# Performance work log

Hardware: AMD Instinct MI355X
Metric: run time of the kernel (lower is better)

Reference implementation:

```python
import jax, jax.numpy as jnp
import numpy as np

EMBED = 768
HEADS = 12
HEAD_DIM = EMBED // HEADS
HIDDEN = 3072
EPS = 1e-5


def setup_inputs() -> dict:
    key = jax.random.key(0)
    ks = jax.random.split(key, 8)
    s = lambda d: 1.0 / np.sqrt(d)
    return {
        "x": jax.random.normal(ks[0], (1, 4096, EMBED), jnp.float32),
        "ln1_w": jnp.ones((EMBED,), jnp.float32),
        "ln1_b": jnp.zeros((EMBED,), jnp.float32),
        "qkv_w": jax.random.normal(ks[1], (3 * EMBED, EMBED), jnp.float32) * s(EMBED),
        "qkv_b": jnp.zeros((3 * EMBED,), jnp.float32),
        "out_w": jax.random.normal(ks[2], (EMBED, EMBED), jnp.float32) * s(EMBED),
        "out_b": jnp.zeros((EMBED,), jnp.float32),
        "ln2_w": jnp.ones((EMBED,), jnp.float32),
        "ln2_b": jnp.zeros((EMBED,), jnp.float32),
        "fc1_w": jax.random.normal(ks[3], (HIDDEN, EMBED), jnp.float32) * s(EMBED),
        "fc1_b": jnp.zeros((HIDDEN,), jnp.float32),
        "fc2_w": jax.random.normal(ks[4], (EMBED, HIDDEN), jnp.float32) * s(HIDDEN),
        "fc2_b": jnp.zeros((EMBED,), jnp.float32),
    }


def _layernorm(x, w, b):
    mu = jnp.mean(x, axis=-1, keepdims=True)
    var = jnp.mean(jnp.square(x - mu), axis=-1, keepdims=True)
    return (x - mu) * jax.lax.rsqrt(var + EPS) * w + b


def reference(x, ln1_w, ln1_b, qkv_w, qkv_b, out_w, out_b,
              ln2_w, ln2_b, fc1_w, fc1_b, fc2_w, fc2_b):
    B, N, _ = x.shape
    # attention branch
    h = _layernorm(x, ln1_w, ln1_b)
    qkv = h @ qkv_w.T + qkv_b                      # [B,N,3E]
    qkv = qkv.reshape(B, N, 3, HEADS, HEAD_DIM)
    q = jnp.transpose(qkv[:, :, 0], (0, 2, 1, 3))  # [B,H,N,D]
    k = jnp.transpose(qkv[:, :, 1], (0, 2, 1, 3))
    v = jnp.transpose(qkv[:, :, 2], (0, 2, 1, 3))
    scores = jnp.einsum("bhqd,bhkd->bhqk", q, k) / np.sqrt(HEAD_DIM)
    probs = jax.nn.softmax(scores, axis=-1)
    attn = jnp.einsum("bhqk,bhkd->bhqd", probs, v)
    attn = jnp.transpose(attn, (0, 2, 1, 3)).reshape(B, N, EMBED)
    x = x + (attn @ out_w.T + out_b)
    # mlp branch
    h = _layernorm(x, ln2_w, ln2_b)
    h = jax.nn.gelu(h @ fc1_w.T + fc1_b, approximate=False)
    x = x + (h @ fc2_w.T + fc2_b)
    return x
```

## Files before the change

kernel.cpp:

```cpp
#include <hip/hip_runtime.h>
#include <hip/hip_bf16.h>

#define SEQ  4096
#define EMB  768
#define NH   12
#define HD   64
#define HID  3072
#define QKVC 2304

typedef __attribute__((ext_vector_type(8))) short bf16x8;
typedef __attribute__((ext_vector_type(4))) float f32x4;

#define MFMA16(a,b,c) __builtin_amdgcn_mfma_f32_16x16x32_bf16(a,b,c,0,0,0)

#define QSCL 0.18033688f

__device__ __forceinline__ unsigned short f2bf(float f){
  union { float f; unsigned u; } c; c.f = f;
  unsigned r = c.u + 0x7FFFu + ((c.u >> 16) & 1u);
  return (unsigned short)(r >> 16);
}

__device__ __forceinline__ float bf2f(unsigned short u){
  union { unsigned u; float f; } c; c.u = (unsigned)u << 16; return c.f;
}

__device__ __forceinline__ unsigned cvtpk(float a, float b){
  unsigned r;
  asm("v_cvt_pk_bf16_f32 %0, %1, %2" : "=v"(r) : "v"(a), "v"(b));
  return r;
}

__device__ __forceinline__ float gelu_f(float x){
  float x2 = x * x;
  float u  = __builtin_amdgcn_exp2f(x * fmaf(x2, 0.1029433f, 2.3022082f));
  return x * u * __builtin_amdgcn_rcpf(1.f + u);
}

__device__ __forceinline__ void gload_lds16(const unsigned short* g, unsigned short* l){
  __builtin_amdgcn_global_load_lds(
      (const __attribute__((address_space(1))) unsigned int*)g,
      (__attribute__((address_space(3))) unsigned int*)l, 16, 0, 0);
}

__global__ void cvt4_kernel(const float* __restrict__ s0, unsigned short* __restrict__ d0, int n0,
                            const float* __restrict__ s1, unsigned short* __restrict__ d1, int n1,
                            const float* __restrict__ s2, unsigned short* __restrict__ d2, int n2,
                            const float* __restrict__ s3, unsigned short* __restrict__ d3, int n3){
  long e = ((long)blockIdx.x * 256 + threadIdx.x) << 2;
  const float* s; unsigned short* d;
  if (e < n0){ s = s0; d = d0; }
  else if ((e -= n0) < n1){ s = s1; d = d1; }
  else if ((e -= n1) < n2){ s = s2; d = d2; }
  else if ((e -= n2) < n3){ s = s3; d = d3; }
  else return;
  float4 v = *(const float4*)(s + e);
  ushort4 u;
  u.x = f2bf(v.x); u.y = f2bf(v.y); u.z = f2bf(v.z); u.w = f2bf(v.w);
  *(ushort4*)(d + e) = u;
}

__global__ __launch_bounds__(256) void ln_kernel(const float* __restrict__ x,
    const float* __restrict__ w, const float* __restrict__ b,
    unsigned short* __restrict__ out)
{
  const int row = blockIdx.x;
  const float* xr = x + (size_t)row * EMB;
  const int t = threadIdx.x;
  float v0 = xr[t], v1 = xr[t + 256], v2 = xr[t + 512];
  float s  = v0 + v1 + v2;
  float s2 = v0*v0 + v1*v1 + v2*v2;
  #pragma unroll
  for (int off = 32; off; off >>= 1){ s += __shfl_down(s, off); s2 += __shfl_down(s2, off); }
  __shared__ float rs[4], rq[4], st[2];
  int wv = t >> 6;
  if ((t & 63) == 0){ rs[wv] = s; rq[wv] = s2; }
  __syncthreads();
  if (t == 0){
    float S  = rs[0] + rs[1] + rs[2] + rs[3];
    float S2 = rq[0] + rq[1] + rq[2] + rq[3];
    float mu  = S * (1.f / 768.f);
    float var = S2 * (1.f / 768.f) - mu * mu;
    st[0] = mu; st[1] = rsqrtf(var + 1e-5f);
  }
  __syncthreads();
  float mu = st[0], rstd = st[1];
  unsigned short* orow = out + (size_t)row * EMB;
  orow[t]       = f2bf((v0 - mu) * rstd * w[t]       + b[t]);
  orow[t + 256] = f2bf((v1 - mu) * rstd * w[t + 256] + b[t + 256]);
  orow[t + 512] = f2bf((v2 - mu) * rstd * w[t + 512] + b[t + 512]);
}

template<int EPI, int BM, int BN, int BK>
__global__ __launch_bounds__(256, (BM == 64 ? 4 : 3)) void gemm_kernel(
    const unsigned short* __restrict__ A, const unsigned short* __restrict__ B,
    const float* __restrict__ bias, const float* __restrict__ res,
    unsigned short* __restrict__ Ob, float* __restrict__ Of,
    int M, int N, int K)
{
  constexpr int MF  = BM / 32;
  constexpr int NF  = BN / 32;
  constexpr int KS  = BK / 32;
  constexpr int CPR = BK / 8;
  constexpr int AIT = BM * BK / 2048;
  constexpr int BIT = BN * BK / 2048;
  __shared__ unsigned short sA[2][BM * BK];
  __shared__ unsigned short sB[2][BN * BK];
  const int tid  = threadIdx.x;
  const int w    = tid >> 6, lane = tid & 63;
  const int wr   = w >> 1,   wc   = w & 1;
  const int l15  = lane & 15, l4  = lane >> 4;
  const int tm   = blockIdx.y, tn = blockIdx.x;
  const unsigned short* Ab = A + (size_t)tm * BM * K;
  const unsigned short* Bb = B + (size_t)tn * BN * K;

  f32x4 acc[MF][NF];
  #pragma unroll
  for (int m = 0; m < MF; ++m)
    #pragma unroll
    for (int n = 0; n < NF; ++n){ acc[m][n][0]=0.f; acc[m][n][1]=0.f; acc[m][n][2]=0.f; acc[m][n][3]=0.f; }

  #define GSTAGE(buf, kt) { \
    const int k0_ = (kt) * BK; \
    _Pragma("unroll") \
    for (int i = 0; i < AIT; ++i){ \
      int c = i * 256 + tid; int row = c / CPR; int skc = (c % CPR) ^ (row & (CPR - 1)); \
      gload_lds16(Ab + (size_t)row * K + k0_ + skc * 8, &sA[buf][(i * 256 + w * 64) * 8]); } \
    _Pragma("unroll") \
    for (int i = 0; i < BIT; ++i){ \
      int c = i * 256 + tid; int row = c / CPR; int skc = (c % CPR) ^ (row & (CPR - 1)); \
      gload_lds16(Bb + (size_t)row * K + k0_ + skc * 8, &sB[buf][(i * 256 + w * 64) * 8]); }}

  #define GCOMPUTE(buf) { \
    _Pragma("unroll") \
    for (int ks = 0; ks < KS; ++ks){ \
      bf16x8 af[MF], bg[NF]; \
      _Pragma("unroll") \
      for (int m = 0; m < MF; ++m){ \
        int row = wr * (BM / 2) + m * 16 + l15; \
        int kc  = ks * 4 + l4; \
        af[m] = *(const bf16x8*)&sA[buf][row * BK + ((kc ^ (row & (CPR - 1))) << 3)]; } \
      _Pragma("unroll") \
      for (int n = 0; n < NF; ++n){ \
        int row = wc * (BN / 2) + n * 16 + l15; \
        int kc  = ks * 4 + l4; \
        bg[n] = *(const bf16x8*)&sB[buf][row * BK + ((kc ^ (row & (CPR - 1))) << 3)]; } \
      _Pragma("unroll") \
      for (int m = 0; m < MF; ++m) \
        _Pragma("unroll") \
        for (int n = 0; n < NF; ++n) \
          acc[m][n] = MFMA16(af[m], bg[n], acc[m][n]); }}

  const int nk = K / BK;
  GSTAGE(0, 0);
  int cur = 0;
  for (int kt = 0; kt < nk; ++kt){
    __syncthreads();
    if (kt + 1 < nk) GSTAGE(cur ^ 1, kt + 1);
    GCOMPUTE(cur);
    cur ^= 1;
  }
  #undef GSTAGE
  #undef GCOMPUTE

  #pragma unroll
  for (int m = 0; m < MF; ++m){
    int row0 = tm * BM + wr * (BM / 2) + m * 16 + l4 * 4;
    #pragma unroll
    for (int n = 0; n < NF; ++n){
      int col = tn * BN + wc * (BN / 2) + n * 16 + l15;
      float bv = bias[col];
      #pragma unroll
      for (int r = 0; r < 4; ++r){
        int row = row0 + r;
        float v = acc[m][n][r] + bv;
        if (EPI == 0){
          Ob[(size_t)row * N + col] = f2bf(v);
        } else if (EPI == 1){
          Ob[(size_t)row * N + col] = f2bf(gelu_f(v));
        } else if (EPI == 3){
          if (col < EMB) v *= QSCL;
          Ob[(size_t)row * N + col] = f2bf(v);
        } else {
          v += res[(size_t)row * N + col];
          Of[(size_t)row * N + col] = v;
        }
      }
    }
  }
}

__global__ __launch_bounds__(256, 3) void attn_kernel(
    const unsigned short* __restrict__ qkv,
    unsigned short* __restrict__ pO, float2* __restrict__ pml)
{
  __shared__ unsigned short sK[2][64 * 64];
  __shared__ unsigned short sVt[2][64 * 64];
  __shared__ unsigned short sEp[4][16 * 72];
  const int tid = threadIdx.x, w = tid >> 6, lane = tid & 63;
  const int l15 = lane & 15, l4 = lane >> 4;

  const int bid  = blockIdx.x;
  const int v_id = (bid & 7) * 96 + (bid >> 3);
  const int head = v_id >> 6;
  const int r6   = v_id & 63;
  const int qt   = r6 >> 1;
  const int sk   = r6 & 1;

  const int koff = EMB + head * HD;
  const int voff = 2 * EMB + head * HD;
  const int qbase = qt * 128 + w * 32;
  const int tbase = sk * 32;

  bf16x8 qf[2][2];
  #pragma unroll
  for (int qg = 0; qg < 2; ++qg){
    const unsigned short* qp = qkv + (size_t)(qbase + qg * 16 + l15) * QKVC + head * HD + l4 * 8;
    qf[qg][0] = *(const bf16x8*)qp;
    qf[qg][1] = *(const bf16x8*)(qp + 32);
  }

  f32x4 oaccT[4][2];
  #pragma unroll
  for (int i = 0; i < 4; ++i)
    #pragma unroll
    for (int qg = 0; qg < 2; ++qg){ oaccT[i][qg][0]=0.f; oaccT[i][qg][1]=0.f; oaccT[i][qg][2]=0.f; oaccT[i][qg][3]=0.f; }
  float m0 = -3.0e38f, m1 = -3.0e38f, l0 = 0.f, l1 = 0.f;

  const int krow = tid >> 3;
  const int kskc = (tid & 7) ^ (krow & 7);
  const int vp_  = tid >> 3;
  const int d0   = (tid & 7) * 8;
  const int w16  = vp_ & 15;
  const int qpos = (w16 & 1) | (((w16 >> 3) & 1) << 1) | (((w16 >> 1) & 3) << 2);
  const int Pc   = ((vp_ >> 4) << 2) | (qpos >> 2);
  const int Ps   = qpos & 3;

  #define KSTAGE(buf, t) { \
    const int kv0_ = (t) << 6; \
    gload_lds16(qkv + (size_t)(kv0_ + krow) * QKVC + koff + kskc * 8,      &sK[buf][(w * 64) * 8]); \
    gload_lds16(qkv + (size_t)(kv0_ + 32 + krow) * QKVC + koff + kskc * 8, &sK[buf][(256 + w * 64) * 8]); }

  #define VLOAD(t) { \
    const unsigned short* vp = qkv + (size_t)(((t) << 6) + vp_ * 2) * QKVC + voff + d0; \
    va = *(const bf16x8*)vp; \
    vb = *(const bf16x8*)(vp + QKVC); }

  #define VCOMMIT(buf) { \
    _Pragma("unroll") \
    for (int i = 0; i < 8; ++i){ \
      unsigned pk = (unsigned)(unsigned short)va[i] | ((unsigned)(unsigned short)vb[i] << 16); \
      *(unsigned*)&sVt[buf][(d0 + i) * 64 + ((Pc ^ (tid & 7) ^ i) << 3) + Ps * 2] = pk; \
    } }

  bf16x8 va, vb;
  KSTAGE(0, tbase);
  VLOAD(tbase);
  VCOMMIT(0);

  for (int tt = 0; tt < 32; ++tt){
    const int cur = tt & 1;
    __syncthreads();
    const bool pre = (tt < 31);
    if (pre){
      KSTAGE(cur ^ 1, tbase + tt + 1);
      VLOAD(tbase + tt + 1);
    }

    f32x4 sf[4][2];
    #pragma unroll
    for (int i = 0; i < 4; ++i)
      #pragma unroll
      for (int qg = 0; qg < 2; ++qg){ sf[i][qg][0]=0.f; sf[i][qg][1]=0.f; sf[i][qg][2]=0.f; sf[i][qg][3]=0.f; }
    __builtin_amdgcn_s_setprio(1);
    #pragma unroll
    for (int ks = 0; ks < 2; ++ks){
      bf16x8 kf[4];
      #pragma unroll
      for (int nb = 0; nb < 4; ++nb){
        int row = 16 * nb + l15;
        kf[nb] = *(const bf16x8*)&sK[cur][(row * 8 + ((4 * ks + l4) ^ (row & 7))) * 8];
      }
      #pragma unroll
      for (int nb = 0; nb < 4; ++nb){
        sf[nb][0] = MFMA16(kf[nb], qf[0][ks], sf[nb][0]);
        sf[nb][1] = MFMA16(kf[nb], qf[1][ks], sf[nb][1]);
      }
    }
    __builtin_amdgcn_s_setprio(0);

    float mx0, mx1;
    {
      float a = sf[0][0][0], b = sf[0][1][0];
      #pragma unroll
      for (int nb = 0; nb < 4; ++nb)
        #pragma unroll
        for (int r = 0; r < 4; ++r){
          a = fmaxf(a, sf[nb][0][r]);
          b = fmaxf(b, sf[nb][1][r]);
        }
      a = fmaxf(a, __shfl_xor(a, 16)); a = fmaxf(a, __shfl_xor(a, 32));
      b = fmaxf(b, __shfl_xor(b, 16)); b = fmaxf(b, __shfl_xor(b, 32));
      mx0 = a; mx1 = b;
    }
    bool ok = (mx0 <= m0 + 8.f) && (mx1 <= m1 + 8.f);
    if (!__all(ok)){
      float nm0 = fmaxf(m0, mx0), nm1 = fmaxf(m1, mx1);
      float c0 = __builtin_amdgcn_exp2f(m0 - nm0);
      float c1 = __builtin_amdgcn_exp2f(m1 - nm1);
      m0 = nm0; m1 = nm1; l0 *= c0; l1 *= c1;
      #pragma unroll
      for (int db = 0; db < 4; ++db)
        #pragma unroll
        for (int r = 0; r < 4; ++r){ oaccT[db][0][r] *= c0; oaccT[db][1][r] *= c1; }
    }
    unsigned pbw[2][2][4];
    {
      float ps0 = 0.f, ps1 = 0.f;
      #pragma unroll
      for (int nb = 0; nb < 4; ++nb){
        float p0[4], p1[4];
        #pragma unroll
        for (int r = 0; r < 4; ++r){
          p0[r] = __builtin_amdgcn_exp2f(sf[nb][0][r] - m0); ps0 += p0[r];
          p1[r] = __builtin_amdgcn_exp2f(sf[nb][1][r] - m1); ps1 += p1[r];
        }
        pbw[0][nb >> 1][(nb & 1) * 2]     = cvtpk(p0[0], p0[1]);
        pbw[0][nb >> 1][(nb & 1) * 2 + 1] = cvtpk(p0[2], p0[3]);
        pbw[1][nb >> 1][(nb & 1) * 2]     = cvtpk(p1[0], p1[1]);
        pbw[1][nb >> 1][(nb & 1) * 2 + 1] = cvtpk(p1[2], p1[3]);
      }
      ps0 += __shfl_xor(ps0, 16); ps0 += __shfl_xor(ps0, 32);
      ps1 += __shfl_xor(ps1, 16); ps1 += __shfl_xor(ps1, 32);
      l0 += ps0; l1 += ps1;
    }

    __builtin_amdgcn_s_setprio(1);
    {
      bf16x8 vv[2][4];
      #pragma unroll
      for (int ks = 0; ks < 2; ++ks)
        #pragma unroll
        for (int db = 0; db < 4; ++db){
          int d = 16 * db + l15;
          int cp = (4 * ks + l4) ^ ((d >> 3) & 7) ^ (d & 7);
          vv[ks][db] = *(const bf16x8*)&sVt[cur][d * 64 + cp * 8];
        }
      union { unsigned uw[4]; bf16x8 v; } pb;
      #pragma unroll
      for (int qg = 0; qg < 2; ++qg){
        bf16x8 pb0, pb1;
        pb.uw[0]=pbw[qg][0][0]; pb.uw[1]=pbw[qg][0][1]; pb.uw[2]=pbw[qg][0][2]; pb.uw[3]=pbw[qg][0][3]; pb0 = pb.v;
        pb.uw[0]=pbw[qg][1][0]; pb.uw[1]=pbw[qg][1][1]; pb.uw[2]=pbw[qg][1][2]; pb.uw[3]=pbw[qg][1][3]; pb1 = pb.v;
        #pragma unroll
        for (int db = 0; db < 4; ++db){
          oaccT[db][qg] = MFMA16(vv[0][db], pb0, oaccT[db][qg]);
          oaccT[db][qg] = MFMA16(vv[1][db], pb1, oaccT[db][qg]);
        }
      }
    }
    __builtin_amdgcn_s_setprio(0);

    if (pre) VCOMMIT(cur ^ 1);
  }

  #pragma unroll
  for (int qg = 0; qg < 2; ++qg){
    unsigned short* sPw = sEp[w];
    #pragma unroll
    for (int db = 0; db < 4; ++db)
      #pragma unroll
      for (int dw = 0; dw < 2; ++dw){
        unsigned pk = cvtpk(oaccT[db][qg][2 * dw], oaccT[db][qg][2 * dw + 1]);
        *(unsigned*)&sPw[l15 * 72 + 16 * db + 4 * l4 + 2 * dw] = pk;
      }
    int qe = lane >> 2, de = (lane & 3) * 16;
    bf16x8 r0 = *(const bf16x8*)&sPw[qe * 72 + de];
    bf16x8 r1 = *(const bf16x8*)&sPw[qe * 72 + de + 8];
    unsigned short* op = pO + ((size_t)(sk * NH + head) * SEQ + qbase + qg * 16 + qe) * 64 + de;
    *(bf16x8*)op = r0;
    *(bf16x8*)(op + 8) = r1;
  }
  if (lane < 16){
    size_t r = (size_t)(sk * NH + head) * SEQ + qbase + l15;
    pml[r]      = make_float2(m0, l0);
    pml[r + 16] = make_float2(m1, l1);
  }
  #undef KSTAGE
  #undef VLOAD
  #undef VCOMMIT
}

__global__ __launch_bounds__(256) void comb_kernel(
    const unsigned short* __restrict__ pO, const float2* __restrict__ pml,
    unsigned short* __restrict__ o)
{
  const int t = threadIdx.x;
  const int row = blockIdx.x * 64 + (t >> 2);
  const int dseg = (t & 3) * 16;
  float2 a = pml[row], b = pml[NH * SEQ + row];
  float M = fmaxf(a.x, b.x);
  float c0 = __builtin_amdgcn_exp2f(a.x - M);
  float c1 = __builtin_amdgcn_exp2f(b.x - M);
  float inv = 1.f / (c0 * a.y + c1 * b.y);
  c0 *= inv; c1 *= inv;
  const unsigned short* p0 = pO + (size_t)row * 64 + dseg;
  const unsigned short* p1 = p0 + (size_t)NH * SEQ * 64;
  bf16x8 x0 = *(const bf16x8*)p0, x1 = *(const bf16x8*)(p0 + 8);
  bf16x8 y0 = *(const bf16x8*)p1, y1 = *(const bf16x8*)(p1 + 8);
  const int head = row >> 12, q = row & (SEQ - 1);
  unsigned short* op = o + (size_t)q * EMB + head * HD + dseg;
  union { unsigned uw[4]; bf16x8 v; } r0, r1;
  #pragma unroll
  for (int i = 0; i < 4; ++i){
    r0.uw[i] = cvtpk(c0 * bf2f((unsigned short)x0[2*i])   + c1 * bf2f((unsigned short)y0[2*i]),
                     c0 * bf2f((unsigned short)x0[2*i+1]) + c1 * bf2f((unsigned short)y0[2*i+1]));
    r1.uw[i] = cvtpk(c0 * bf2f((unsigned short)x1[2*i])   + c1 * bf2f((unsigned short)y1[2*i]),
                     c0 * bf2f((unsigned short)x1[2*i+1]) + c1 * bf2f((unsigned short)y1[2*i+1]));
  }
  *(bf16x8*)op = r0.v;
  *(bf16x8*)(op + 8) = r1.v;
}

extern "C" void kernel_launch(void* const* d_in, const int* in_sizes, int n_in,
                              void* d_out, int out_size, void* d_ws, size_t ws_size,
                              hipStream_t stream)
{
  const float* x    = (const float*)d_in[0];
  const float* ln1w = (const float*)d_in[1];
  const float* ln1b = (const float*)d_in[2];
  const float* qkvw = (const float*)d_in[3];
  const float* qkvb = (const float*)d_in[4];
  const float* outw = (const float*)d_in[5];
  const float* outb = (const float*)d_in[6];
  const float* ln2w = (const float*)d_in[7];
  const float* ln2b = (const float*)d_in[8];
  const float* fc1w = (const float*)d_in[9];
  const float* fc1b = (const float*)d_in[10];
  const float* fc2w = (const float*)d_in[11];
  const float* fc2b = (const float*)d_in[12];
  float* out = (float*)d_out;

  char* ws = (char*)d_ws;
  unsigned short* wqkv = (unsigned short*)ws; ws += (size_t)QKVC * EMB * 2;
  unsigned short* wout = (unsigned short*)ws; ws += (size_t)EMB * EMB * 2;
  unsigned short* wfc1 = (unsigned short*)ws; ws += (size_t)HID * EMB * 2;
  unsigned short* wfc2 = (unsigned short*)ws; ws += (size_t)EMB * HID * 2;
  unsigned short* h1   = (unsigned short*)ws; ws += (size_t)SEQ * EMB * 2;
  unsigned short* qkv  = (unsigned short*)ws; ws += (size_t)SEQ * QKVC * 2;
  unsigned short* h3   = (unsigned short*)ws; ws += (size_t)SEQ * HID * 2;
  unsigned short* attnb = h1;
  unsigned short* h2    = qkv;
  unsigned short* pO  = h3;
  float2*         pml = (float2*)(h3 + (size_t)2 * NH * SEQ * 64);

  const int n0 = QKVC * EMB, n1 = EMB * EMB, n2 = HID * EMB, n3 = EMB * HID;
  cvt4_kernel<<<(n0 + n1 + n2 + n3) / 4 / 256, 256, 0, stream>>>(
      qkvw, wqkv, n0, outw, wout, n1, fc1w, wfc1, n2, fc2w, wfc2, n3);

  ln_kernel<<<SEQ, 256, 0, stream>>>(x, ln1w, ln1b, h1);

  gemm_kernel<3, 128, 128, 32><<<dim3(QKVC / 128, SEQ / 128), 256, 0, stream>>>(
      h1, wqkv, qkvb, nullptr, qkv, nullptr, SEQ, QKVC, EMB);

  attn_kernel<<<SEQ / 128 * NH * 2, 256, 0, stream>>>(qkv, pO, pml);
  comb_kernel<<<NH * SEQ / 64, 256, 0, stream>>>(pO, pml, attnb);

  gemm_kernel<2, 64, 64, 64><<<dim3(EMB / 64, SEQ / 64), 256, 0, stream>>>(
      attnb, wout, outb, x, nullptr, out, SEQ, EMB, EMB);

  ln_kernel<<<SEQ, 256, 0, stream>>>(out, ln2w, ln2b, h2);

  gemm_kernel<1, 128, 128, 32><<<dim3(HID / 128, SEQ / 128), 256, 0, stream>>>(
      h2, wfc1, fc1b, nullptr, h3, nullptr, SEQ, HID, EMB);

  gemm_kernel<2, 64, 64, 64><<<dim3(EMB / 64, SEQ / 64), 256, 0, stream>>>(
      h3, wfc2, fc2b, out, nullptr, out, SEQ, EMB, HID);
}
```

Baseline: 210.4 us.

## Fuse LN1 with weight conversion, triple-buffer large GEMMs, use max3 in attention

Merges the first layernorm and the fp32-to-bf16 weight conversion into a single launch, dropping one kernel launch and letting the two independent jobs run side by side. The 128x128 GEMMs move to a three-stage LDS ring with explicit vmcnt waits, so two tiles are in flight while one is computed. The attention row-max reduction uses v_max3_f32 to roughly halve the max instructions. The triple buffer raises LDS use per block, which may reduce occupancy, and the hand-written vmcnt(4) count depends on GSTAGE issuing exactly four loads per stage.

```diff
diff --git a/kernel.cpp b/kernel.cpp
--- a/kernel.cpp
+++ b/kernel.cpp
@@ -31,6 +31,12 @@
   return r;
 }
 
+__device__ __forceinline__ float fmax3(float a, float b, float c){
+  float r;
+  asm("v_max3_f32 %0, %1, %2, %3" : "=v"(r) : "v"(a), "v"(b), "v"(c));
+  return r;
+}
+
 __device__ __forceinline__ float gelu_f(float x){
   float x2 = x * x;
   float u  = __builtin_amdgcn_exp2f(x * fmaf(x2, 0.1029433f, 2.3022082f));
@@ -43,21 +49,53 @@
       (__attribute__((address_space(3))) unsigned int*)l, 16, 0, 0);
 }
 
-__global__ void cvt4_kernel(const float* __restrict__ s0, unsigned short* __restrict__ d0, int n0,
-                            const float* __restrict__ s1, unsigned short* __restrict__ d1, int n1,
-                            const float* __restrict__ s2, unsigned short* __restrict__ d2, int n2,
-                            const float* __restrict__ s3, unsigned short* __restrict__ d3, int n3){
-  long e = ((long)blockIdx.x * 256 + threadIdx.x) << 2;
-  const float* s; unsigned short* d;
-  if (e < n0){ s = s0; d = d0; }
-  else if ((e -= n0) < n1){ s = s1; d = d1; }
-  else if ((e -= n1) < n2){ s = s2; d = d2; }
-  else if ((e -= n2) < n3){ s = s3; d = d3; }
-  else return;
-  float4 v = *(const float4*)(s + e);
-  ushort4 u;
-  u.x = f2bf(v.x); u.y = f2bf(v.y); u.z = f2bf(v.z); u.w = f2bf(v.w);
-  *(ushort4*)(d + e) = u;
+__global__ __launch_bounds__(256) void pre_kernel(
+    const float* __restrict__ x, const float* __restrict__ w, const float* __restrict__ b,
+    unsigned short* __restrict__ out,
+    const float* __restrict__ s0, unsigned short* __restrict__ d0, int n0,
+    const float* __restrict__ s1, unsigned short* __restrict__ d1, int n1,
+    const float* __restrict__ s2, unsigned short* __restrict__ d2, int n2,
+    const float* __restrict__ s3, unsigned short* __restrict__ d3, int n3)
+{
+  const int t = threadIdx.x;
+  if (blockIdx.x < SEQ){
+    const int row = blockIdx.x;
+    const float* xr = x + (size_t)row * EMB;
+    float v0 = xr[t], v1 = xr[t + 256], v2 = xr[t + 512];
+    float s  = v0 + v1 + v2;
+    float s2 = v0*v0 + v1*v1 + v2*v2;
+    #pragma unroll
+    for (int off = 32; off; off >>= 1){ s += __shfl_down(s, off); s2 += __shfl_down(s2, off); }
+    __shared__ float rs[4], rq[4], st[2];
+    int wv = t >> 6;
+    if ((t & 63) == 0){ rs[wv] = s; rq[wv] = s2; }
+    __syncthreads();
+    if (t == 0){
+      float S  = rs[0] + rs[1] + rs[2] + rs[3];
+      float S2 = rq[0] + rq[1] + rq[2] + rq[3];
+      float mu  = S * (1.f / 768.f);
+      float var = S2 * (1.f / 768.f) - mu * mu;
+      st[0] = mu; st[1] = rsqrtf(var + 1e-5f);
+    }
+    __syncthreads();
+    float mu = st[0], rstd = st[1];
+    unsigned short* orow = out + (size_t)row * EMB;
+    orow[t]       = f2bf((v0 - mu) * rstd * w[t]       + b[t]);
+    orow[t + 256] = f2bf((v1 - mu) * rstd * w[t + 256] + b[t + 256]);
+    orow[t + 512] = f2bf((v2 - mu) * rstd * w[t + 512] + b[t + 512]);
+  } else {
+    long e = ((long)(blockIdx.x - SEQ) * 256 + t) << 2;
+    const float* s; unsigned short* d;
+    if (e < n0){ s = s0; d = d0; }
+    else if ((e -= n0) < n1){ s = s1; d = d1; }
+    else if ((e -= n1) < n2){ s = s2; d = d2; }
+    else if ((e -= n2) < n3){ s = s3; d = d3; }
+    else return;
+    float4 v = *(const float4*)(s + e);
+    ushort4 u;
+    u.x = f2bf(v.x); u.y = f2bf(v.y); u.z = f2bf(v.z); u.w = f2bf(v.w);
+    *(ushort4*)(d + e) = u;
+  }
 }
 
 __global__ __launch_bounds__(256) void ln_kernel(const float* __restrict__ x,
@@ -104,8 +142,10 @@
   constexpr int CPR = BK / 8;
   constexpr int AIT = BM * BK / 2048;
   constexpr int BIT = BN * BK / 2048;
-  __shared__ unsigned short sA[2][BM * BK];
-  __shared__ unsigned short sB[2][BN * BK];
+  constexpr bool CNT = (BM == 128);
+  constexpr int NBUF = CNT ? 3 : 2;
+  __shared__ unsigned short sA[NBUF][BM * BK];
+  __shared__ unsigned short sB[NBUF][BN * BK];
   const int tid  = threadIdx.x;
   const int w    = tid >> 6, lane = tid & 63;
   const int wr   = w >> 1,   wc   = w & 1;
@@ -152,13 +192,25 @@
           acc[m][n] = MFMA16(af[m], bg[n], acc[m][n]); }}
 
   const int nk = K / BK;
-  GSTAGE(0, 0);
-  int cur = 0;
-  for (int kt = 0; kt < nk; ++kt){
-    __syncthreads();
-    if (kt + 1 < nk) GSTAGE(cur ^ 1, kt + 1);
-    GCOMPUTE(cur);
-    cur ^= 1;
+  if (CNT){
+    GSTAGE(0, 0);
+    GSTAGE(1, 1);
+    for (int kt = 0; kt < nk; ++kt){
+      if (kt + 2 < nk) asm volatile("s_waitcnt vmcnt(4)" ::: "memory");
+      else             asm volatile("s_waitcnt vmcnt(0)" ::: "memory");
+      __builtin_amdgcn_s_barrier();
+      if (kt + 2 < nk) GSTAGE((kt + 2) % 3, kt + 2);
+      GCOMPUTE(kt % 3);
+    }
+  } else {
+    GSTAGE(0, 0);
+    int cur = 0;
+    for (int kt = 0; kt < nk; ++kt){
+      __syncthreads();
+      if (kt + 1 < nk) GSTAGE(cur ^ 1, kt + 1);
+      GCOMPUTE(cur);
+      cur ^= 1;
+    }
   }
   #undef GSTAGE
   #undef GCOMPUTE
@@ -292,13 +344,14 @@
     float mx0, mx1;
     {
       float a = sf[0][0][0], b = sf[0][1][0];
-      #pragma unroll
-      for (int nb = 0; nb < 4; ++nb)
-        #pragma unroll
-        for (int r = 0; r < 4; ++r){
-          a = fmaxf(a, sf[nb][0][r]);
-          b = fmaxf(b, sf[nb][1][r]);
-        }
+      a = fmax3(a, sf[0][0][1], sf[0][0][2]);  b = fmax3(b, sf[0][1][1], sf[0][1][2]);
+      a = fmax3(a, sf[0][0][3], sf[1][0][0]);  b = fmax3(b, sf[0][1][3], sf[1][1][0]);
+      a = fmax3(a, sf[1][0][1], sf[1][0][2]);  b = fmax3(b, sf[1][1][1], sf[1][1][2]);
+      a = fmax3(a, sf[1][0][3], sf[2][0][0]);  b = fmax3(b, sf[1][1][3], sf[2][1][0]);
+      a = fmax3(a, sf[2][0][1], sf[2][0][2]);  b = fmax3(b, sf[2][1][1], sf[2][1][2]);
+      a = fmax3(a, sf[2][0][3], sf[3][0][0]);  b = fmax3(b, sf[2][1][3], sf[3][1][0]);
+      a = fmax3(a, sf[3][0][1], sf[3][0][2]);  b = fmax3(b, sf[3][1][1], sf[3][1][2]);
+      a = fmaxf(a, sf[3][0][3]);               b = fmaxf(b, sf[3][1][3]);
       a = fmaxf(a, __shfl_xor(a, 16)); a = fmaxf(a, __shfl_xor(a, 32));
       b = fmaxf(b, __shfl_xor(b, 16)); b = fmaxf(b, __shfl_xor(b, 32));
       mx0 = a; mx1 = b;
@@ -455,10 +508,9 @@
   float2*         pml = (float2*)(h3 + (size_t)2 * NH * SEQ * 64);
 
   const int n0 = QKVC * EMB, n1 = EMB * EMB, n2 = HID * EMB, n3 = EMB * HID;
-  cvt4_kernel<<<(n0 + n1 + n2 + n3) / 4 / 256, 256, 0, stream>>>(
+  pre_kernel<<<SEQ + (n0 + n1 + n2 + n3) / 4 / 256, 256, 0, stream>>>(
+      x, ln1w, ln1b, h1,
       qkvw, wqkv, n0, outw, wout, n1, fc1w, wfc1, n2, fc2w, wfc2, n3);
-
-  ln_kernel<<<SEQ, 256, 0, stream>>>(x, ln1w, ln1b, h1);
 
   gemm_kernel<3, 128, 128, 32><<<dim3(QKVC / 128, SEQ / 128), 256, 0, stream>>>(
       h1, wqkv, qkvb, nullptr, qkv, nullptr, SEQ, QKVC, EMB);
```

After: 209.0 us. Within noise of the previous version (-0.7%).
